# Kernel tuning notes

Hardware: AMD Instinct MI355X
Metric: run time of the kernel (lower is better)

The kernel has to match this reference:

```python
import jax, jax.numpy as jnp
from jax import lax
import numpy as np

GAMMA = 0.999
LAM = 0.95
ENTROPY_COEFF = 0.01

T = 4096
N_ENVS = 1024


def setup_inputs() -> dict:
    key = jax.random.key(0)
    k1, k2, k3, k4, k5 = jax.random.split(key, 5)
    return {
        "ep_rewards": jax.random.normal(k1, (T, N_ENVS), dtype=jnp.float32),
        "ep_log_probs": jax.random.normal(k2, (T, N_ENVS), dtype=jnp.float32),
        "ep_value_preds": jax.random.normal(k3, (T, N_ENVS), dtype=jnp.float32),
        "last_value_pred": jax.random.normal(k4, (N_ENVS, 1), dtype=jnp.float32),
        "ep_entropies": jax.random.uniform(k5, (T, N_ENVS), dtype=jnp.float32),
        "ep_masks": jnp.ones((T, N_ENVS), dtype=jnp.float32),
    }


def reference(ep_rewards, ep_log_probs, ep_value_preds, last_value_pred,
              ep_entropies, ep_masks):
    # value_preds extended with bootstrap value: [T+1, n_envs]
    v_ext = jnp.concatenate(
        [ep_value_preds, lax.stop_gradient(last_value_pred.T)], axis=0)

    def step(next_adv, inp):
        r, v_next, v, m = inp
        ret = r + GAMMA * v_next * m
        td = ret - v
        adv = td + GAMMA * LAM * next_adv * m
        return adv, (ret, adv)

    init = jnp.zeros_like(ep_rewards[0])  # [n_envs]
    _, (returns, advantages) = lax.scan(
        step, init,
        (ep_rewards, v_ext[1:], v_ext[:-1], ep_masks),
        reverse=True)

    critic_loss = jnp.mean(advantages ** 2)
    actor_loss = (-jnp.mean(ep_log_probs * lax.stop_gradient(advantages))
                  - ENTROPY_COEFF * jnp.mean(ep_entropies))
    return critic_loss, actor_loss
```

## Files before the change

### kernel.cpp

```cpp
#include <hip/hip_runtime.h>
#include <math.h>

#define GAMMA 0.999f
#define LAM   0.95f
#define GL    (GAMMA * LAM)

constexpr int T    = 4096;
constexpr int NENV = 1024;

struct Seg { float P, Q, s2, spq, sq2, slpp, slpq; };

__device__ __forceinline__ Seg seg_combine(const Seg& A, const Seg& B) {
    Seg r;
    const float qb = B.Q, pb = B.P;
    r.s2   = B.s2 + A.s2 + 2.f * A.spq * pb + A.sq2 * pb * pb;
    r.spq  = B.spq + (A.spq + A.sq2 * pb) * qb;
    r.sq2  = B.sq2 + A.sq2 * qb * qb;
    r.slpp = B.slpp + A.slpp + A.slpq * pb;
    r.slpq = B.slpq + A.slpq * qb;
    r.P    = A.P + A.Q * pb;
    r.Q    = A.Q * qb;
    return r;
}

__global__ __launch_bounds__(256) void gae_pass1(
    const float* __restrict__ R, const float* __restrict__ LP,
    const float* __restrict__ V, const float* __restrict__ LV,
    const float* __restrict__ E, const float* __restrict__ M,
    float* __restrict__ summ, float* __restrict__ entp, int C, int L)
{
    const int c    = blockIdx.x >> 1;
    const int env  = 2 * ((blockIdx.x & 1) * 256 + threadIdx.x);
    const int t_lo = c * L;
    const int t_hi = t_lo + L - 1;

    float2 vn = (c == C - 1) ? *(const float2*)(LV + env)
                             : *(const float2*)(V + (size_t)(t_hi + 1) * NENV + env);

    float p0=0.f,q0=1.f,s20=0.f,spq0=0.f,sq20=0.f,slpp0=0.f,slpq0=0.f;
    float p1=0.f,q1=1.f,s21=0.f,spq1=0.f,sq21=0.f,slpp1=0.f,slpq1=0.f;
    float sent = 0.f;

    #pragma unroll 4
    for (int t = t_hi; t >= t_lo; --t) {
        const size_t idx = (size_t)t * NENV + env;
        const float2 r  = *(const float2*)(R  + idx);
        const float2 v  = *(const float2*)(V  + idx);
        const float2 m  = *(const float2*)(M  + idx);
        const float2 lp = *(const float2*)(LP + idx);
        const float2 e  = *(const float2*)(E  + idx);

        float ret = fmaf(GAMMA * vn.x, m.x, r.x);
        float a   = ret - v.x;
        float b   = GL * m.x;
        p0 = fmaf(b, p0, a); q0 = b * q0;
        s20 = fmaf(p0, p0, s20); spq0 = fmaf(p0, q0, spq0); sq20 = fmaf(q0, q0, sq20);
        slpp0 = fmaf(lp.x, p0, slpp0); slpq0 = fmaf(lp.x, q0, slpq0);

        ret = fmaf(GAMMA * vn.y, m.y, r.y);
        a   = ret - v.y;
        b   = GL * m.y;
        p1 = fmaf(b, p1, a); q1 = b * q1;
        s21 = fmaf(p1, p1, s21); spq1 = fmaf(p1, q1, spq1); sq21 = fmaf(q1, q1, sq21);
        slpp1 = fmaf(lp.y, p1, slpp1); slpq1 = fmaf(lp.y, q1, slpq1);

        sent += e.x + e.y;
        vn = v;
    }

    float4* s0 = (float4*)(summ + ((size_t)env * C + c) * 8);
    s0[0] = make_float4(p0, q0, s20, spq0);
    s0[1] = make_float4(sq20, slpp0, slpq0, 0.f);
    float4* s1 = (float4*)(summ + ((size_t)(env + 1) * C + c) * 8);
    s1[0] = make_float4(p1, q1, s21, spq1);
    s1[1] = make_float4(sq21, slpp1, slpq1, 0.f);

    #pragma unroll
    for (int o = 32; o > 0; o >>= 1) sent += __shfl_down(sent, o, 64);
    __shared__ float ls[4];
    const int lane = threadIdx.x & 63, w = threadIdx.x >> 6;
    if (lane == 0) ls[w] = sent;
    __syncthreads();
    if (threadIdx.x == 0) entp[blockIdx.x] = (ls[0] + ls[1]) + (ls[2] + ls[3]);
}

__global__ __launch_bounds__(256) void gae_pass2(
    const float* __restrict__ summ, float* __restrict__ part, int C)
{
    const int lane = threadIdx.x & 63;
    const int env  = blockIdx.x * 4 + (threadIdx.x >> 6);
    const int K    = C >> 6;
    const int c_hi = C - 1 - lane * K;

    const float* base = summ + ((size_t)env * C + c_hi) * 8;
    float4 a0 = ((const float4*)base)[0];
    float4 a1 = ((const float4*)base)[1];
    Seg cur = { a0.x, a0.y, a0.z, a0.w, a1.x, a1.y, a1.z };

    for (int j = 1; j < K; ++j) {
        const float* b = summ + ((size_t)env * C + (c_hi - j)) * 8;
        float4 b0 = ((const float4*)b)[0];
        float4 b1 = ((const float4*)b)[1];
        Seg A = { b0.x, b0.y, b0.z, b0.w, b1.x, b1.y, b1.z };
        cur = seg_combine(A, cur);
    }

    #pragma unroll
    for (int d = 1; d < 64; d <<= 1) {
        Seg o;
        o.P    = __shfl_down(cur.P,    d, 64);
        o.Q    = __shfl_down(cur.Q,    d, 64);
        o.s2   = __shfl_down(cur.s2,   d, 64);
        o.spq  = __shfl_down(cur.spq,  d, 64);
        o.sq2  = __shfl_down(cur.sq2,  d, 64);
        o.slpp = __shfl_down(cur.slpp, d, 64);
        o.slpq = __shfl_down(cur.slpq, d, 64);
        cur = seg_combine(o, cur);
    }

    if (lane == 0) {
        part[env * 2 + 0] = cur.s2;
        part[env * 2 + 1] = cur.slpp;
    }
}

__global__ __launch_bounds__(256) void gae_pass3(
    const float* __restrict__ part, const float* __restrict__ entp,
    int nent, float* __restrict__ out)
{
    const int tid = threadIdx.x;
    float crit = 0.f, act = 0.f, ent = 0.f;
    for (int i = tid; i < NENV; i += 256) {
        crit += part[2 * i + 0];
        act  += part[2 * i + 1];
    }
    for (int i = tid; i < nent; i += 256) ent += entp[i];

    #pragma unroll
    for (int o = 32; o > 0; o >>= 1) {
        crit += __shfl_down(crit, o, 64);
        act  += __shfl_down(act,  o, 64);
        ent  += __shfl_down(ent,  o, 64);
    }
    __shared__ float lc[4], la[4], le[4];
    const int lane = tid & 63, w = tid >> 6;
    if (lane == 0) { lc[w] = crit; la[w] = act; le[w] = ent; }
    __syncthreads();
    if (tid == 0) {
        crit = (lc[0] + lc[1]) + (lc[2] + lc[3]);
        act  = (la[0] + la[1]) + (la[2] + la[3]);
        ent  = (le[0] + le[1]) + (le[2] + le[3]);
        const float inv = 1.f / (float)((size_t)T * NENV);
        out[0] = crit * inv;
        out[1] = -act * inv - 0.01f * (ent * inv);
    }
}

extern "C" void kernel_launch(void* const* d_in, const int* in_sizes, int n_in,
                              void* d_out, int out_size, void* d_ws, size_t ws_size,
                              hipStream_t stream) {
    const float* R  = (const float*)d_in[0];
    const float* LP = (const float*)d_in[1];
    const float* V  = (const float*)d_in[2];
    const float* LV = (const float*)d_in[3];
    const float* E  = (const float*)d_in[4];
    const float* M  = (const float*)d_in[5];
    float* out = (float*)d_out;

    int C = 256;
    while (C > 64) {
        size_t need = ((size_t)C * 8 * NENV + (size_t)C * 2 + 2 * NENV) * sizeof(float);
        if (need <= ws_size) break;
        C >>= 1;
    }
    const int L = T / C;

    float* summ = (float*)d_ws;
    float* entp = summ + (size_t)C * 8 * NENV;
    float* part = entp + (size_t)C * 2;

    gae_pass1<<<C * 2, 256, 0, stream>>>(R, LP, V, LV, E, M, summ, entp, C, L);
    gae_pass2<<<NENV / 4, 256, 0, stream>>>(summ, part, C);
    gae_pass3<<<1, 256, 0, stream>>>(part, entp, C * 2, out);
}
```

Before: 28.68 us.

## Fuse final reduction into pass2 via last-block atomic counter, fix C=512

Removes the third kernel launch by having the last block of pass2, found with an atomic counter, perform the final reduction. The chunk count is fixed at compile time to 512 (shorter per-chunk scan of 8 steps, more blocks in pass1), which lets the time loop and the pass2 combine loop unroll fully. The counter is reset inside pass1. The change drops the workspace-size check, so it relies on the workspace being large enough for 512 chunks, and the larger summary array raises pass1 write traffic.

```diff
diff --git a/kernel.cpp b/kernel.cpp
--- a/kernel.cpp
+++ b/kernel.cpp
@@ -7,6 +7,8 @@
 
 constexpr int T    = 4096;
 constexpr int NENV = 1024;
+constexpr int C    = 512;
+constexpr int L    = T / C;
 
 struct Seg { float P, Q, s2, spq, sq2, slpp, slpq; };
 
@@ -27,8 +29,11 @@
     const float* __restrict__ R, const float* __restrict__ LP,
     const float* __restrict__ V, const float* __restrict__ LV,
     const float* __restrict__ E, const float* __restrict__ M,
-    float* __restrict__ summ, float* __restrict__ entp, int C, int L)
+    float* __restrict__ summ, float* __restrict__ entp,
+    unsigned int* __restrict__ cnt)
 {
+    if (blockIdx.x == 0 && threadIdx.x == 0) *cnt = 0u;
+
     const int c    = blockIdx.x >> 1;
     const int env  = 2 * ((blockIdx.x & 1) * 256 + threadIdx.x);
     const int t_lo = c * L;
@@ -41,7 +46,7 @@
     float p1=0.f,q1=1.f,s21=0.f,spq1=0.f,sq21=0.f,slpp1=0.f,slpq1=0.f;
     float sent = 0.f;
 
-    #pragma unroll 4
+    #pragma unroll
     for (int t = t_hi; t >= t_lo; --t) {
         const size_t idx = (size_t)t * NENV + env;
         const float2 r  = *(const float2*)(R  + idx);
@@ -85,10 +90,14 @@
 }
 
 __global__ __launch_bounds__(256) void gae_pass2(
-    const float* __restrict__ summ, float* __restrict__ part, int C)
+    const float* __restrict__ summ, const float* __restrict__ entp,
+    float* __restrict__ part, unsigned int* __restrict__ cnt,
+    float* __restrict__ out)
 {
-    const int lane = threadIdx.x & 63;
-    const int env  = blockIdx.x * 4 + (threadIdx.x >> 6);
+    const int tid  = threadIdx.x;
+    const int lane = tid & 63;
+    const int w    = tid >> 6;
+    const int env  = blockIdx.x * 4 + w;
     const int K    = C >> 6;
     const int c_hi = C - 1 - lane * K;
 
@@ -97,10 +106,11 @@
     float4 a1 = ((const float4*)base)[1];
     Seg cur = { a0.x, a0.y, a0.z, a0.w, a1.x, a1.y, a1.z };
 
+    #pragma unroll
     for (int j = 1; j < K; ++j) {
-        const float* b = summ + ((size_t)env * C + (c_hi - j)) * 8;
-        float4 b0 = ((const float4*)b)[0];
-        float4 b1 = ((const float4*)b)[1];
+        const float* bp = summ + ((size_t)env * C + (c_hi - j)) * 8;
+        float4 b0 = ((const float4*)bp)[0];
+        float4 b1 = ((const float4*)bp)[1];
         Seg A = { b0.x, b0.y, b0.z, b0.w, b1.x, b1.y, b1.z };
         cur = seg_combine(A, cur);
     }
@@ -119,22 +129,31 @@
     }
 
     if (lane == 0) {
-        part[env * 2 + 0] = cur.s2;
-        part[env * 2 + 1] = cur.slpp;
+        __hip_atomic_store(&part[env * 2 + 0], cur.s2,
+                           __ATOMIC_RELAXED, __HIP_MEMORY_SCOPE_AGENT);
+        __hip_atomic_store(&part[env * 2 + 1], cur.slpp,
+                           __ATOMIC_RELAXED, __HIP_MEMORY_SCOPE_AGENT);
     }
-}
 
-__global__ __launch_bounds__(256) void gae_pass3(
-    const float* __restrict__ part, const float* __restrict__ entp,
-    int nent, float* __restrict__ out)
-{
-    const int tid = threadIdx.x;
+    __shared__ unsigned int slast;
+    __syncthreads();
+    if (tid == 0) {
+        __threadfence();
+        unsigned int o = atomicAdd(cnt, 1u);
+        slast = (o == gridDim.x - 1) ? 1u : 0u;
+    }
+    __syncthreads();
+    if (!slast) return;
+
+    __threadfence();
     float crit = 0.f, act = 0.f, ent = 0.f;
     for (int i = tid; i < NENV; i += 256) {
-        crit += part[2 * i + 0];
-        act  += part[2 * i + 1];
+        crit += __hip_atomic_load(&part[2 * i + 0],
+                                  __ATOMIC_RELAXED, __HIP_MEMORY_SCOPE_AGENT);
+        act  += __hip_atomic_load(&part[2 * i + 1],
+                                  __ATOMIC_RELAXED, __HIP_MEMORY_SCOPE_AGENT);
     }
-    for (int i = tid; i < nent; i += 256) ent += entp[i];
+    for (int i = tid; i < 2 * C; i += 256) ent += entp[i];
 
     #pragma unroll
     for (int o = 32; o > 0; o >>= 1) {
@@ -143,7 +162,6 @@
         ent  += __shfl_down(ent,  o, 64);
     }
     __shared__ float lc[4], la[4], le[4];
-    const int lane = tid & 63, w = tid >> 6;
     if (lane == 0) { lc[w] = crit; la[w] = act; le[w] = ent; }
     __syncthreads();
     if (tid == 0) {
@@ -167,19 +185,11 @@
     const float* M  = (const float*)d_in[5];
     float* out = (float*)d_out;
 
-    int C = 256;
-    while (C > 64) {
-        size_t need = ((size_t)C * 8 * NENV + (size_t)C * 2 + 2 * NENV) * sizeof(float);
-        if (need <= ws_size) break;
-        C >>= 1;
-    }
-    const int L = T / C;
-
     float* summ = (float*)d_ws;
     float* entp = summ + (size_t)C * 8 * NENV;
-    float* part = entp + (size_t)C * 2;
+    float* part = entp + 2 * C;
+    unsigned int* cnt = (unsigned int*)(part + 2 * NENV);
 
-    gae_pass1<<<C * 2, 256, 0, stream>>>(R, LP, V, LV, E, M, summ, entp, C, L);
-    gae_pass2<<<NENV / 4, 256, 0, stream>>>(summ, part, C);
-    gae_pass3<<<1, 256, 0, stream>>>(part, entp, C * 2, out);
+    gae_pass1<<<C * 2, 256, 0, stream>>>(R, LP, V, LV, E, M, summ, entp, cnt);
+    gae_pass2<<<NENV / 4, 256, 0, stream>>>(summ, entp, part, cnt, out);
 }
```

Measured after the change: 36.83 us. 1.28x slower.
